# Kernel optimization log

Hardware: AMD Instinct MI355X
Metric: run time of the kernel (lower is better)

Reference implementation:

```python
import jax, jax.numpy as jnp
import numpy as np
import math

B, S, A, E = 64, 8, 128, 256
H = 4
D = E // H  # head_dim = 64


def setup_inputs() -> dict:
    key = jax.random.key(0)
    ks = jax.random.split(key, 10)
    scale = 1.0 / math.sqrt(E)
    return {
        "predicate_emb": jax.random.normal(ks[0], (B, S, A, 1, E), jnp.float32),
        "constant_embs": jax.random.normal(ks[1], (B, S, A, 2, E), jnp.float32),
        "Wq": jax.random.normal(ks[2], (E, E), jnp.float32) * scale,
        "bq": jax.random.normal(ks[3], (E,), jnp.float32) * scale,
        "Wk": jax.random.normal(ks[4], (E, E), jnp.float32) * scale,
        "bk": jax.random.normal(ks[5], (E,), jnp.float32) * scale,
        "Wv": jax.random.normal(ks[6], (E, E), jnp.float32) * scale,
        "bv": jax.random.normal(ks[7], (E,), jnp.float32) * scale,
        "Wo": jax.random.normal(ks[8], (E, E), jnp.float32) * scale,
        "bo": jax.random.normal(ks[9], (E,), jnp.float32) * scale,
    }


def reference(predicate_emb, constant_embs, Wq, bq, Wk, bk, Wv, bv, Wo, bo):
    # dropout_rate = 0.0 -> dropout is identity
    p = predicate_emb[..., 0, :]                       # [B,S,A,E]  (squeeze(3))
    Q = p @ Wq.T + bq                                  # [B,S,A,E]
    K = constant_embs @ Wk.T + bk                      # [B,S,A,2,E]
    V = constant_embs @ Wv.T + bv                      # [B,S,A,2,E]

    Qh = Q.reshape(B, S, A, H, D)                      # [B,S,A,H,D]
    Kh = K.reshape(B, S, A, 2, H, D)                   # [B,S,A,2,H,D]
    Vh = V.reshape(B, S, A, 2, H, D)

    inv_sqrt_d = 1.0 / math.sqrt(D)
    # scores over the 2 keys per (atom, head)
    scores = jnp.einsum('bsahd,bsakhd->bsahk', Qh, Kh) * inv_sqrt_d  # [B,S,A,H,2]
    attn = jax.nn.softmax(scores, axis=-1)                            # [B,S,A,H,2]
    ws = jnp.einsum('bsahk,bsakhd->bsahd', attn, Vh)                  # [B,S,A,H,D]

    concat = ws.reshape(B, S, A, E)
    return concat @ Wo.T + bo                           # [B,S,A,E]
```

## Files before the change

kernel.cpp:

```cpp
#include <hip/hip_runtime.h>

#define LSTR 264

typedef short short4v __attribute__((ext_vector_type(4)));
typedef short short8v __attribute__((ext_vector_type(8)));
typedef float f32x4 __attribute__((ext_vector_type(4)));

#define MFMA(a, b, c) __builtin_amdgcn_mfma_f32_16x16x32_bf16((a), (b), (c), 0, 0, 0)

__device__ __forceinline__ short f2bf(float f) {
  unsigned u = __float_as_uint(f);
  unsigned r = u + 0x7fffu + ((u >> 16) & 1u);
  return (short)(r >> 16);
}

__device__ __forceinline__ short4v f2bf4(float4 v) {
  short4v s;
  s.x = f2bf(v.x); s.y = f2bf(v.y); s.z = f2bf(v.z); s.w = f2bf(v.w);
  return s;
}


__global__ __launch_bounds__(256) void prep1_kernel(
    const float* __restrict__ Wv, const float* __restrict__ Wo,
    const float* __restrict__ bv, const float* __restrict__ bo,
    short* __restrict__ pvo, float* __restrict__ bvo) {
  __shared__ float srow[256];
  __shared__ float red[256];
  const int n = blockIdx.x, k = threadIdx.x;
  const float wov = Wo[n * 256 + k];
  srow[k] = wov;
  red[k] = wov * bv[k];
  __syncthreads();
  float acc = 0.f;
#pragma unroll 16
  for (int j = 0; j < 256; ++j) acc += srow[j] * Wv[j * 256 + k];
  const int h = n >> 6, nt = (n >> 4) & 3, col = n & 15;
  const int ks = k >> 5, quad = (k >> 3) & 3, j8 = k & 7;
  pvo[h * 16384 + (ks * 4 + nt) * 512 + (quad * 16 + col) * 8 + j8] = f2bf(acc);
  for (int s = 128; s > 0; s >>= 1) {
    if (k < s) red[k] += red[k + s];
    __syncthreads();
  }
  if (k == 0) bvo[n] = red[0] + bo[n];
}

__global__ __launch_bounds__(256) void pack_kernel(
    const float* __restrict__ Wq, const float* __restrict__ Wk,
    const float* __restrict__ Wv, const float* __restrict__ Wo,
    short* __restrict__ pq, short* __restrict__ pk,
    short* __restrict__ pv, short* __restrict__ po) {
  const int g = blockIdx.x * 256 + threadIdx.x;
  const int n = g >> 5;
  const int c8 = g & 31;
  const int h = n >> 6, nt = (n >> 4) & 3, col = n & 15;
  const int ks = c8 >> 2, quad = c8 & 3;
  const int src = n * 256 + c8 * 8;
  const int dst = h * 16384 + (ks * 4 + nt) * 512 + (quad * 16 + col) * 8;
  const float4* q4 = (const float4*)(Wq + src);
  const float4* k4 = (const float4*)(Wk + src);
  const float4* v4 = (const float4*)(Wv + src);
  const float4* o4 = (const float4*)(Wo + src);
  float4 qa = q4[0], qb = q4[1], ka = k4[0], kb = k4[1];
  float4 va = v4[0], vb = v4[1], oa = o4[0], ob = o4[1];
  *(short4v*)(pq + dst) = f2bf4(qa); *(short4v*)(pq + dst + 4) = f2bf4(qb);
  *(short4v*)(pk + dst) = f2bf4(ka); *(short4v*)(pk + dst + 4) = f2bf4(kb);
  *(short4v*)(pv + dst) = f2bf4(va); *(short4v*)(pv + dst + 4) = f2bf4(vb);
  *(short4v*)(po + dst) = f2bf4(oa); *(short4v*)(po + dst + 4) = f2bf4(ob);
}

__device__ __forceinline__ void gemm_qk(const short* Ap, const short* Ad,
                                        const short* __restrict__ wq,
                                        const short* __restrict__ wk,
                                        int col, int quad,
                                        f32x4 accQ[2][4], f32x4 accK[2][4]) {
  const short* p0 = Ap + col * LSTR + quad * 8;
  const short* p1 = p0 + 16 * LSTR;
  const short* d0 = Ad + col * LSTR + quad * 8;
  const short* d1 = d0 + 16 * LSTR;
  short8v ap0 = *(const short8v*)p0;
  short8v ap1 = *(const short8v*)p1;
  short8v ad0 = *(const short8v*)d0;
  short8v ad1 = *(const short8v*)d1;
  short8v qb0 = *(const short8v*)(wq);
  short8v qb1 = *(const short8v*)(wq + 512);
  short8v qb2 = *(const short8v*)(wq + 1024);
  short8v kb0 = *(const short8v*)(wk);
  short8v kb1 = *(const short8v*)(wk + 512);
  short8v kb2 = *(const short8v*)(wk + 1024);
#pragma unroll
  for (int ks = 0; ks < 8; ++ks) {
    const int kn = (ks + 1) & 7;
    short8v ap0n = *(const short8v*)(p0 + kn * 32);
    short8v ap1n = *(const short8v*)(p1 + kn * 32);
    short8v ad0n = *(const short8v*)(d0 + kn * 32);
    short8v ad1n = *(const short8v*)(d1 + kn * 32);
#pragma unroll
    for (int nt = 0; nt < 4; ++nt) {
      const int f = ks * 4 + nt;
      short8v qbn = *(const short8v*)(wq + ((f + 3) & 31) * 512);
      short8v kbn = *(const short8v*)(wk + ((f + 3) & 31) * 512);
      accQ[0][nt] = MFMA(ap0, qb0, accQ[0][nt]);
      accQ[1][nt] = MFMA(ap1, qb0, accQ[1][nt]);
      accK[0][nt] = MFMA(ad0, kb0, accK[0][nt]);
      accK[1][nt] = MFMA(ad1, kb0, accK[1][nt]);
      qb0 = qb1; qb1 = qb2; qb2 = qbn;
      kb0 = kb1; kb1 = kb2; kb2 = kbn;
    }
    ap0 = ap0n; ap1 = ap1n; ad0 = ad0n; ad1 = ad1n;
  }
}

__device__ __forceinline__ void gemm_v(const short* A, const short* __restrict__ wb,
                                       int col, int quad, f32x4 acc[2][4]) {
  const short* a0p = A + col * LSTR + quad * 8;
  const short* a1p = a0p + 16 * LSTR;
  short8v a0c = *(const short8v*)a0p;
  short8v a1c = *(const short8v*)a1p;
  short8v b0 = *(const short8v*)(wb);
  short8v b1 = *(const short8v*)(wb + 512);
  short8v b2 = *(const short8v*)(wb + 1024);
  short8v b3 = *(const short8v*)(wb + 1536);
#pragma unroll
  for (int ks = 0; ks < 8; ++ks) {
    const int kn = (ks + 1) & 7;
    short8v a0n = *(const short8v*)(a0p + kn * 32);
    short8v a1n = *(const short8v*)(a1p + kn * 32);
#pragma unroll
    for (int nt = 0; nt < 4; ++nt) {
      const int f = ks * 4 + nt;
      short8v bn = *(const short8v*)(wb + ((f + 4) & 31) * 512);
      acc[0][nt] = MFMA(a0c, b0, acc[0][nt]);
      acc[1][nt] = MFMA(a1c, b0, acc[1][nt]);
      b0 = b1; b1 = b2; b2 = b3; b3 = bn;
    }
    a0c = a0n; a1c = a1n;
  }
}

__device__ __forceinline__ void gemm_o(const short* Ac, const short* Ag,
                                       const short* __restrict__ wvo,
                                       const short* __restrict__ wo,
                                       int col, int quad,
                                       f32x4 accA[2][4], f32x4 accB[2][4]) {
  const short* c0p = Ac + col * LSTR + quad * 8;
  const short* c1p = c0p + 16 * LSTR;
  const short* g0p = Ag + col * LSTR + quad * 8;
  const short* g1p = g0p + 16 * LSTR;
  short8v ac0 = *(const short8v*)c0p;
  short8v ac1 = *(const short8v*)c1p;
  short8v ag0 = *(const short8v*)g0p;
  short8v ag1 = *(const short8v*)g1p;
  short8v vb0 = *(const short8v*)(wvo);
  short8v vb1 = *(const short8v*)(wvo + 512);
  short8v vb2 = *(const short8v*)(wvo + 1024);
  short8v ob0 = *(const short8v*)(wo);
  short8v ob1 = *(const short8v*)(wo + 512);
  short8v ob2 = *(const short8v*)(wo + 1024);
#pragma unroll
  for (int ks = 0; ks < 8; ++ks) {
    const int kn = (ks + 1) & 7;
    short8v ac0n = *(const short8v*)(c0p + kn * 32);
    short8v ac1n = *(const short8v*)(c1p + kn * 32);
    short8v ag0n = *(const short8v*)(g0p + kn * 32);
    short8v ag1n = *(const short8v*)(g1p + kn * 32);
#pragma unroll
    for (int nt = 0; nt < 4; ++nt) {
      const int f = ks * 4 + nt;
      short8v vbn = *(const short8v*)(wvo + ((f + 3) & 31) * 512);
      short8v obn = *(const short8v*)(wo + ((f + 3) & 31) * 512);
      accA[0][nt] = MFMA(ac0, vb0, accA[0][nt]);
      accA[1][nt] = MFMA(ac1, vb0, accA[1][nt]);
      accB[0][nt] = MFMA(ag0, ob0, accB[0][nt]);
      accB[1][nt] = MFMA(ag1, ob0, accB[1][nt]);
      vb0 = vb1; vb1 = vb2; vb2 = vbn;
      ob0 = ob1; ob1 = ob2; ob2 = obn;
    }
    ac0 = ac0n; ac1 = ac1n; ag0 = ag0n; ag1 = ag1n;
  }
}

__global__ __launch_bounds__(256, 3) void fused_kernel(
    const float* __restrict__ pred, const float* __restrict__ cemb,
    const short* __restrict__ pq, const short* __restrict__ pk,
    const short* __restrict__ pv, const short* __restrict__ po,
    const short* __restrict__ pvo, const float* __restrict__ bq,
    const float* __restrict__ bvo, float* __restrict__ out) {
  __shared__ __align__(16) short bufP[32 * LSTR];
  __shared__ __align__(16) short bufD[32 * LSTR];
  __shared__ __align__(16) short bufC1[32 * LSTR];
  const int tid = threadIdx.x;
  const size_t t0 = (size_t)blockIdx.x * 32;

  {
    const int r = tid >> 3;
    const int c0 = tid & 7;
    const float4* prow = (const float4*)(pred + (t0 + r) * 256);
    const float4* crow = (const float4*)(cemb + (t0 + r) * 512);
    float4 pv_[8], av[8], bw[8];
#pragma unroll
    for (int i = 0; i < 8; ++i) pv_[i] = prow[c0 + 8 * i];
#pragma unroll
    for (int i = 0; i < 8; ++i) av[i] = crow[c0 + 8 * i];
#pragma unroll
    for (int i = 0; i < 8; ++i) bw[i] = crow[64 + c0 + 8 * i];
    short* pd = bufP + r * LSTR;
    short* dd = bufD + r * LSTR;
    short* cd = bufC1 + r * LSTR;
#pragma unroll
    for (int i = 0; i < 8; ++i) {
      const int j = c0 + 8 * i;
      *(short4v*)(pd + 4 * j) = f2bf4(pv_[i]);
      float4 d4 = make_float4(av[i].x - bw[i].x, av[i].y - bw[i].y,
                              av[i].z - bw[i].z, av[i].w - bw[i].w);
      *(short4v*)(dd + 4 * j) = f2bf4(d4);
      *(short4v*)(cd + 4 * j) = f2bf4(bw[i]);
    }
  }
  __syncthreads();

  const int lane = tid & 63;
  const int w = tid >> 6;
  const int col = lane & 15;
  const int quad = lane >> 4;
  const int nbase = w * 64;
  const int woff = w * 16384 + lane * 8;

  float bqv[4];
#pragma unroll
  for (int nt = 0; nt < 4; ++nt) bqv[nt] = bq[nbase + nt * 16 + col];

  f32x4 accQ[2][4] = {};
  f32x4 accK[2][4] = {};
  gemm_qk(bufP, bufD, pq + woff, pk + woff, col, quad, accQ, accK);

  float g[2][4];
#pragma unroll
  for (int ms = 0; ms < 2; ++ms) {
#pragma unroll
    for (int r = 0; r < 4; ++r) {
      float zz = 0.f;
#pragma unroll
      for (int nt = 0; nt < 4; ++nt)
        zz += (accQ[ms][nt][r] + bqv[nt]) * accK[ms][nt][r];
      zz += __shfl_xor(zz, 1);
      zz += __shfl_xor(zz, 2);
      zz += __shfl_xor(zz, 4);
      zz += __shfl_xor(zz, 8);
      g[ms][r] = 1.f / (1.f + __expf(-0.125f * zz));
    }
  }

  f32x4 accV[2][4] = {};
  gemm_v(bufD, pv + woff, col, quad, accV);

  __syncthreads();
#pragma unroll
  for (int ms = 0; ms < 2; ++ms)
#pragma unroll
    for (int nt = 0; nt < 4; ++nt)
#pragma unroll
      for (int r = 0; r < 4; ++r)
        bufP[(ms * 16 + quad * 4 + r) * LSTR + nbase + nt * 16 + col] =
            f2bf(g[ms][r] * accV[ms][nt][r]);
  __syncthreads();

  float bov[4];
#pragma unroll
  for (int nt = 0; nt < 4; ++nt) bov[nt] = bvo[nbase + nt * 16 + col];

  f32x4 accO1[2][4] = {};
  f32x4 accO2[2][4] = {};
  gemm_o(bufC1, bufP, pvo + woff, po + woff, col, quad, accO1, accO2);

#pragma unroll
  for (int ms = 0; ms < 2; ++ms)
#pragma unroll
    for (int nt = 0; nt < 4; ++nt)
#pragma unroll
      for (int r = 0; r < 4; ++r)
        out[(t0 + ms * 16 + quad * 4 + r) * 256 + nbase + nt * 16 + col] =
            accO1[ms][nt][r] + accO2[ms][nt][r] + bov[nt];
}

extern "C" void kernel_launch(void* const* d_in, const int* in_sizes, int n_in,
                              void* d_out, int out_size, void* d_ws, size_t ws_size,
                              hipStream_t stream) {
  const float* pred = (const float*)d_in[0];
  const float* cemb = (const float*)d_in[1];
  const float* Wq = (const float*)d_in[2];
  const float* bq = (const float*)d_in[3];
  const float* Wk = (const float*)d_in[4];
  const float* Wv = (const float*)d_in[6];
  const float* bv = (const float*)d_in[7];
  const float* Wo = (const float*)d_in[8];
  const float* bo = (const float*)d_in[9];
  float* out = (float*)d_out;

  short* pq = (short*)d_ws;
  short* pk = pq + 65536;
  short* pv = pk + 65536;
  short* po = pv + 65536;
  short* pvo = po + 65536;
  float* bvo = (float*)(pvo + 65536);

  prep1_kernel<<<256, 256, 0, stream>>>(Wv, Wo, bv, bo, pvo, bvo);
  pack_kernel<<<32, 256, 0, stream>>>(Wq, Wk, Wv, Wo, pq, pk, pv, po);
  fused_kernel<<<2048, 256, 0, stream>>>(pred, cemb, pq, pk, pv, po, pvo, bq, bvo, out);
}
```

Before: 329.9 us.

## Persistent multi-tile fused kernel with register prefetch and merged prep kernels

Merges the two weight-prep kernels into one launch, which removes one kernel launch. The fused kernel now processes four 32-row tiles per block, using 512 blocks instead of 2048. The next tile's fp32 inputs are prefetched into registers while the current tile is being computed. Launch bounds drop from 3 to 2 waves per SIMD to make room for the prefetch registers, at the cost of lower occupancy and an added barrier per tile.

Result: slower. 693.1 us (+110.1%).

```diff
diff --git a/kernel.cpp b/kernel.cpp
--- a/kernel.cpp
+++ b/kernel.cpp
@@ -1,6 +1,7 @@
 #include <hip/hip_runtime.h>
 
 #define LSTR 264
+#define TILES 4
 
 typedef short short4v __attribute__((ext_vector_type(4)));
 typedef short short8v __attribute__((ext_vector_type(8)));
@@ -21,52 +22,51 @@
 }
 
 
-__global__ __launch_bounds__(256) void prep1_kernel(
+__global__ __launch_bounds__(256) void prep_kernel(
+    const float* __restrict__ Wq, const float* __restrict__ Wk,
     const float* __restrict__ Wv, const float* __restrict__ Wo,
     const float* __restrict__ bv, const float* __restrict__ bo,
+    short* __restrict__ pq, short* __restrict__ pk,
+    short* __restrict__ pv, short* __restrict__ po,
     short* __restrict__ pvo, float* __restrict__ bvo) {
   __shared__ float srow[256];
   __shared__ float red[256];
-  const int n = blockIdx.x, k = threadIdx.x;
-  const float wov = Wo[n * 256 + k];
-  srow[k] = wov;
-  red[k] = wov * bv[k];
-  __syncthreads();
-  float acc = 0.f;
+  if (blockIdx.x < 256) {
+    const int n = blockIdx.x, k = threadIdx.x;
+    const float wov = Wo[n * 256 + k];
+    srow[k] = wov;
+    red[k] = wov * bv[k];
+    __syncthreads();
+    float acc = 0.f;
 #pragma unroll 16
-  for (int j = 0; j < 256; ++j) acc += srow[j] * Wv[j * 256 + k];
-  const int h = n >> 6, nt = (n >> 4) & 3, col = n & 15;
-  const int ks = k >> 5, quad = (k >> 3) & 3, j8 = k & 7;
-  pvo[h * 16384 + (ks * 4 + nt) * 512 + (quad * 16 + col) * 8 + j8] = f2bf(acc);
-  for (int s = 128; s > 0; s >>= 1) {
-    if (k < s) red[k] += red[k + s];
-    __syncthreads();
-  }
-  if (k == 0) bvo[n] = red[0] + bo[n];
-}
-
-__global__ __launch_bounds__(256) void pack_kernel(
-    const float* __restrict__ Wq, const float* __restrict__ Wk,
-    const float* __restrict__ Wv, const float* __restrict__ Wo,
-    short* __restrict__ pq, short* __restrict__ pk,
-    short* __restrict__ pv, short* __restrict__ po) {
-  const int g = blockIdx.x * 256 + threadIdx.x;
-  const int n = g >> 5;
-  const int c8 = g & 31;
-  const int h = n >> 6, nt = (n >> 4) & 3, col = n & 15;
-  const int ks = c8 >> 2, quad = c8 & 3;
-  const int src = n * 256 + c8 * 8;
-  const int dst = h * 16384 + (ks * 4 + nt) * 512 + (quad * 16 + col) * 8;
-  const float4* q4 = (const float4*)(Wq + src);
-  const float4* k4 = (const float4*)(Wk + src);
-  const float4* v4 = (const float4*)(Wv + src);
-  const float4* o4 = (const float4*)(Wo + src);
-  float4 qa = q4[0], qb = q4[1], ka = k4[0], kb = k4[1];
-  float4 va = v4[0], vb = v4[1], oa = o4[0], ob = o4[1];
-  *(short4v*)(pq + dst) = f2bf4(qa); *(short4v*)(pq + dst + 4) = f2bf4(qb);
-  *(short4v*)(pk + dst) = f2bf4(ka); *(short4v*)(pk + dst + 4) = f2bf4(kb);
-  *(short4v*)(pv + dst) = f2bf4(va); *(short4v*)(pv + dst + 4) = f2bf4(vb);
-  *(short4v*)(po + dst) = f2bf4(oa); *(short4v*)(po + dst + 4) = f2bf4(ob);
+    for (int j = 0; j < 256; ++j) acc += srow[j] * Wv[j * 256 + k];
+    const int h = n >> 6, nt = (n >> 4) & 3, col = n & 15;
+    const int ks = k >> 5, quad = (k >> 3) & 3, j8 = k & 7;
+    pvo[h * 16384 + (ks * 4 + nt) * 512 + (quad * 16 + col) * 8 + j8] = f2bf(acc);
+    for (int s = 128; s > 0; s >>= 1) {
+      if (k < s) red[k] += red[k + s];
+      __syncthreads();
+    }
+    if (k == 0) bvo[n] = red[0] + bo[n];
+  } else {
+    const int g = (blockIdx.x - 256) * 256 + threadIdx.x;
+    const int n = g >> 5;
+    const int c8 = g & 31;
+    const int h = n >> 6, nt = (n >> 4) & 3, col = n & 15;
+    const int ks = c8 >> 2, quad = c8 & 3;
+    const int src = n * 256 + c8 * 8;
+    const int dst = h * 16384 + (ks * 4 + nt) * 512 + (quad * 16 + col) * 8;
+    const float4* q4 = (const float4*)(Wq + src);
+    const float4* k4 = (const float4*)(Wk + src);
+    const float4* v4 = (const float4*)(Wv + src);
+    const float4* o4 = (const float4*)(Wo + src);
+    float4 qa = q4[0], qb = q4[1], ka = k4[0], kb = k4[1];
+    float4 va = v4[0], vb = v4[1], oa = o4[0], ob = o4[1];
+    *(short4v*)(pq + dst) = f2bf4(qa); *(short4v*)(pq + dst + 4) = f2bf4(qb);
+    *(short4v*)(pk + dst) = f2bf4(ka); *(short4v*)(pk + dst + 4) = f2bf4(kb);
+    *(short4v*)(pv + dst) = f2bf4(va); *(short4v*)(pv + dst + 4) = f2bf4(vb);
+    *(short4v*)(po + dst) = f2bf4(oa); *(short4v*)(po + dst + 4) = f2bf4(ob);
+  }
 }
 
 __device__ __forceinline__ void gemm_qk(const short* Ap, const short* Ad,
@@ -180,7 +180,7 @@
   }
 }
 
-__global__ __launch_bounds__(256, 3) void fused_kernel(
+__global__ __launch_bounds__(256, 2) void fused_kernel(
     const float* __restrict__ pred, const float* __restrict__ cemb,
     const short* __restrict__ pq, const short* __restrict__ pk,
     const short* __restrict__ pv, const short* __restrict__ po,
@@ -190,97 +190,113 @@
   __shared__ __align__(16) short bufD[32 * LSTR];
   __shared__ __align__(16) short bufC1[32 * LSTR];
   const int tid = threadIdx.x;
-  const size_t t0 = (size_t)blockIdx.x * 32;
-
-  {
-    const int r = tid >> 3;
-    const int c0 = tid & 7;
-    const float4* prow = (const float4*)(pred + (t0 + r) * 256);
-    const float4* crow = (const float4*)(cemb + (t0 + r) * 512);
-    float4 pv_[8], av[8], bw[8];
-#pragma unroll
-    for (int i = 0; i < 8; ++i) pv_[i] = prow[c0 + 8 * i];
-#pragma unroll
-    for (int i = 0; i < 8; ++i) av[i] = crow[c0 + 8 * i];
-#pragma unroll
-    for (int i = 0; i < 8; ++i) bw[i] = crow[64 + c0 + 8 * i];
-    short* pd = bufP + r * LSTR;
-    short* dd = bufD + r * LSTR;
-    short* cd = bufC1 + r * LSTR;
-#pragma unroll
-    for (int i = 0; i < 8; ++i) {
-      const int j = c0 + 8 * i;
-      *(short4v*)(pd + 4 * j) = f2bf4(pv_[i]);
-      float4 d4 = make_float4(av[i].x - bw[i].x, av[i].y - bw[i].y,
-                              av[i].z - bw[i].z, av[i].w - bw[i].w);
-      *(short4v*)(dd + 4 * j) = f2bf4(d4);
-      *(short4v*)(cd + 4 * j) = f2bf4(bw[i]);
-    }
-  }
-  __syncthreads();
-
   const int lane = tid & 63;
   const int w = tid >> 6;
   const int col = lane & 15;
   const int quad = lane >> 4;
   const int nbase = w * 64;
   const int woff = w * 16384 + lane * 8;
-
-  float bqv[4];
+  const int r = tid >> 3;
+  const int c8 = tid & 7;
+
+  float bqv[4], bov[4];
 #pragma unroll
   for (int nt = 0; nt < 4; ++nt) bqv[nt] = bq[nbase + nt * 16 + col];
-
-  f32x4 accQ[2][4] = {};
-  f32x4 accK[2][4] = {};
-  gemm_qk(bufP, bufD, pq + woff, pk + woff, col, quad, accQ, accK);
-
-  float g[2][4];
-#pragma unroll
-  for (int ms = 0; ms < 2; ++ms) {
-#pragma unroll
-    for (int r = 0; r < 4; ++r) {
-      float zz = 0.f;
+#pragma unroll
+  for (int nt = 0; nt < 4; ++nt) bov[nt] = bvo[nbase + nt * 16 + col];
+
+  float4 pv_[8], av[8], bw[8];
+  {
+    const size_t t0 = (size_t)blockIdx.x * TILES * 32;
+    const float4* prow = (const float4*)(pred + (t0 + r) * 256);
+    const float4* crow = (const float4*)(cemb + (t0 + r) * 512);
+#pragma unroll
+    for (int i = 0; i < 8; ++i) pv_[i] = prow[c8 + 8 * i];
+#pragma unroll
+    for (int i = 0; i < 8; ++i) av[i] = crow[c8 + 8 * i];
+#pragma unroll
+    for (int i = 0; i < 8; ++i) bw[i] = crow[64 + c8 + 8 * i];
+  }
+
+  for (int it = 0; it < TILES; ++it) {
+    const size_t t0 = ((size_t)blockIdx.x * TILES + it) * 32;
+
+    {
+      short* pd = bufP + r * LSTR;
+      short* dd = bufD + r * LSTR;
+      short* cd = bufC1 + r * LSTR;
+#pragma unroll
+      for (int i = 0; i < 8; ++i) {
+        const int j = c8 + 8 * i;
+        *(short4v*)(pd + 4 * j) = f2bf4(pv_[i]);
+        float4 d4 = make_float4(av[i].x - bw[i].x, av[i].y - bw[i].y,
+                                av[i].z - bw[i].z, av[i].w - bw[i].w);
+        *(short4v*)(dd + 4 * j) = f2bf4(d4);
+        *(short4v*)(cd + 4 * j) = f2bf4(bw[i]);
+      }
+    }
+    if (it + 1 < TILES) {
+      const float4* prow = (const float4*)(pred + (t0 + 32 + r) * 256);
+      const float4* crow = (const float4*)(cemb + (t0 + 32 + r) * 512);
+#pragma unroll
+      for (int i = 0; i < 8; ++i) pv_[i] = prow[c8 + 8 * i];
+#pragma unroll
+      for (int i = 0; i < 8; ++i) av[i] = crow[c8 + 8 * i];
+#pragma unroll
+      for (int i = 0; i < 8; ++i) bw[i] = crow[64 + c8 + 8 * i];
+    }
+    __syncthreads();
+
+    f32x4 accQ[2][4] = {};
+    f32x4 accK[2][4] = {};
+    gemm_qk(bufP, bufD, pq + woff, pk + woff, col, quad, accQ, accK);
+
+    float g[2][4];
+#pragma unroll
+    for (int ms = 0; ms < 2; ++ms) {
+#pragma unroll
+      for (int rr = 0; rr < 4; ++rr) {
+        float zz = 0.f;
+#pragma unroll
+        for (int nt = 0; nt < 4; ++nt)
+          zz += (accQ[ms][nt][rr] + bqv[nt]) * accK[ms][nt][rr];
+        zz += __shfl_xor(zz, 1);
+        zz += __shfl_xor(zz, 2);
+        zz += __shfl_xor(zz, 4);
+        zz += __shfl_xor(zz, 8);
+        g[ms][rr] = 1.f / (1.f + __expf(-0.125f * zz));
+      }
+    }
+
+    f32x4 accV[2][4] = {};
+    gemm_v(bufD, pv + woff, col, quad, accV);
+
+    __syncthreads();
+#pragma unroll
+    for (int ms = 0; ms < 2; ++ms)
 #pragma unroll
       for (int nt = 0; nt < 4; ++nt)
-        zz += (accQ[ms][nt][r] + bqv[nt]) * accK[ms][nt][r];
-      zz += __shfl_xor(zz, 1);
-      zz += __shfl_xor(zz, 2);
-      zz += __shfl_xor(zz, 4);
-      zz += __shfl_xor(zz, 8);
-      g[ms][r] = 1.f / (1.f + __expf(-0.125f * zz));
-    }
-  }
-
-  f32x4 accV[2][4] = {};
-  gemm_v(bufD, pv + woff, col, quad, accV);
-
-  __syncthreads();
-#pragma unroll
-  for (int ms = 0; ms < 2; ++ms)
-#pragma unroll
-    for (int nt = 0; nt < 4; ++nt)
-#pragma unroll
-      for (int r = 0; r < 4; ++r)
-        bufP[(ms * 16 + quad * 4 + r) * LSTR + nbase + nt * 16 + col] =
-            f2bf(g[ms][r] * accV[ms][nt][r]);
-  __syncthreads();
-
-  float bov[4];
-#pragma unroll
-  for (int nt = 0; nt < 4; ++nt) bov[nt] = bvo[nbase + nt * 16 + col];
-
-  f32x4 accO1[2][4] = {};
-  f32x4 accO2[2][4] = {};
-  gemm_o(bufC1, bufP, pvo + woff, po + woff, col, quad, accO1, accO2);
-
-#pragma unroll
-  for (int ms = 0; ms < 2; ++ms)
-#pragma unroll
-    for (int nt = 0; nt < 4; ++nt)
-#pragma unroll
-      for (int r = 0; r < 4; ++r)
-        out[(t0 + ms * 16 + quad * 4 + r) * 256 + nbase + nt * 16 + col] =
-            accO1[ms][nt][r] + accO2[ms][nt][r] + bov[nt];
+#pragma unroll
+        for (int rr = 0; rr < 4; ++rr)
+          bufP[(ms * 16 + quad * 4 + rr) * LSTR + nbase + nt * 16 + col] =
+              f2bf(g[ms][rr] * accV[ms][nt][rr]);
+    __syncthreads();
+
+    f32x4 accO1[2][4] = {};
+    f32x4 accO2[2][4] = {};
+    gemm_o(bufC1, bufP, pvo + woff, po + woff, col, quad, accO1, accO2);
+
+#pragma unroll
+    for (int ms = 0; ms < 2; ++ms)
+#pragma unroll
+      for (int nt = 0; nt < 4; ++nt)
+#pragma unroll
+        for (int rr = 0; rr < 4; ++rr)
+          out[(t0 + ms * 16 + quad * 4 + rr) * 256 + nbase + nt * 16 + col] =
+              accO1[ms][nt][rr] + accO2[ms][nt][rr] + bov[nt];
+
+    __syncthreads();
+  }
 }
 
 extern "C" void kernel_launch(void* const* d_in, const int* in_sizes, int n_in,
@@ -304,7 +320,6 @@
   short* pvo = po + 65536;
   float* bvo = (float*)(pvo + 65536);
 
-  prep1_kernel<<<256, 256, 0, stream>>>(Wv, Wo, bv, bo, pvo, bvo);
-  pack_kernel<<<32, 256, 0, stream>>>(Wq, Wk, Wv, Wo, pq, pk, pv, po);
-  fused_kernel<<<2048, 256, 0, stream>>>(pred, cemb, pq, pk, pv, po, pvo, bq, bvo, out);
-}
+  prep_kernel<<<288, 256, 0, stream>>>(Wq, Wk, Wv, Wo, bv, bo, pq, pk, pv, po, pvo, bvo);
+  fused_kernel<<<512, 256, 0, stream>>>(pred, cemb, pq, pk, pv, po, pvo, bq, bvo, out);
+}
```
